# Kernel optimization log

Measured on AMD Instinct MI355X. Metric: run time of the kernel, lower is better.

The kernel has to match this reference:

```python
import jax, jax.numpy as jnp
import numpy as np

COST_CLASS = 1.0
COST_COORD = 1.0
ALPHA = 0.25
GAMMA = 2.0
EPS = 1e-8
B, N = 4, 512


def setup_inputs() -> dict:
    key = jax.random.key(0)
    k1, k2, k3 = jax.random.split(key, 3)
    return {
        "pred_logits": jax.random.normal(k1, (B, N), dtype=jnp.float32),
        "pred_points": jax.random.uniform(k2, (B, N, 2), dtype=jnp.float32),
        "gt_points": jax.random.uniform(k3, (B, N, 2), dtype=jnp.float32),
        "gt_mask": jnp.ones((B, N), dtype=bool),
    }


def _cost_matrix(pred_logits, pred_points, gt_points):
    # focal-style classification cost, depends only on the prediction -> column-constant
    prob = jax.nn.sigmoid(pred_logits)                       # [B, N]
    neg = (1.0 - ALPHA) * prob ** GAMMA * (-jnp.log(1.0 - prob + EPS))
    pos = ALPHA * (1.0 - prob) ** GAMMA * (-jnp.log(prob + EPS))
    cost_class = (pos - neg)[:, :, None]                     # [B, N, 1]
    # L1 cdist between pred_points and gt_points
    cost_coord = jnp.sum(
        jnp.abs(pred_points[:, :, None, :] - gt_points[:, None, :, :]), axis=-1
    )                                                        # [B, N, N]
    return COST_CLASS * cost_class + COST_COORD * cost_coord


def _lsa(cost):
    # Jonker-Volgenant shortest augmenting path (e-maxx Hungarian), square, minimization.
    c = np.asarray(cost, dtype=np.float64)
    n = c.shape[0]
    INF = 1e18
    u = np.zeros(n + 1)
    v = np.zeros(n + 1)
    p = np.zeros(n + 1, dtype=np.int64)   # p[j] = row matched to column j (1-based)
    way = np.zeros(n + 1, dtype=np.int64)
    for i in range(1, n + 1):
        p[0] = i
        j0 = 0
        minv = np.full(n + 1, INF)
        used = np.zeros(n + 1, dtype=bool)
        while True:
            used[j0] = True
            i0 = p[j0]
            cur = c[i0 - 1] - u[i0] - v[1:]
            nu = ~used[1:]
            mv = minv[1:]
            wy = way[1:]
            upd = nu & (cur < mv)
            mv[upd] = cur[upd]
            wy[upd] = j0
            cand = np.where(nu, mv, INF)
            j1 = int(np.argmin(cand)) + 1
            delta = cand[j1 - 1]
            u[p[used]] += delta
            v[used] -= delta
            mv[nu] -= delta
            j0 = j1
            if p[j0] == 0:
                break
        while j0:
            j1 = int(way[j0])
            p[j0] = int(p[j1])
            j0 = j1
    col_of_row = np.empty(n, dtype=np.int64)
    col_of_row[p[1:] - 1] = np.arange(n)
    return np.arange(n), col_of_row


def reference(pred_logits, pred_points, gt_points, gt_mask):
    C = _cost_matrix(pred_logits, pred_points, gt_points)   # [B, N, N]
    mask = np.asarray(gt_mask)
    assert mask.all(), "reference assumes all gt slots valid (static shapes)"
    Cn = np.asarray(jax.device_get(C))
    pred_idx, gt_idx = [], []
    for b in range(Cn.shape[0]):
        r, c = _lsa(Cn[b])
        pred_idx.append(r)
        gt_idx.append(c)
    pred_idx = jnp.asarray(np.stack(pred_idx))
    gt_idx = jnp.asarray(np.stack(gt_idx))
    return pred_idx, gt_idx, C
```

## Files before the change

### kernel.cpp

```cpp
#include <hip/hip_runtime.h>
#include <math.h>

constexpr int B_ = 4;
constexpr int N_ = 512;

__device__ __forceinline__ float cephes_expf(float xin) {
#pragma clang fp contract(off)
    float x = fminf(xin, 88.3762626647950f);
    x = fmaxf(x, -88.3762626647949f);
    float fx = x * 1.44269504088896341f;
    fx = fx + 0.5f;
    fx = floorf(fx);
    float tmp = fx * 0.693359375f;
    float z0  = fx * -2.12194440e-4f;
    float r = x - tmp;
    r = r - z0;
    float zz = r * r;
    float y = 1.9875691500E-4f;
    y = y * r + 1.3981999507E-3f;
    y = y * r + 8.3334519073E-3f;
    y = y * r + 4.1665795894E-2f;
    y = y * r + 1.6666665459E-1f;
    y = y * r + 5.0000001201E-1f;
    y = y * zz + r;
    y = y + 1.0f;
    int n = (int)fx;
    float p2n = __uint_as_float((unsigned)(n + 0x7f) << 23);
    float res = y * p2n;
    return fmaxf(res, xin);
}

__device__ __forceinline__ float cephes_logf(float t) {
#pragma clang fp contract(off)
    float xx = fmaxf(t, 1.17549435e-38f);
    unsigned u = __float_as_uint(xx);
    int e_i = (int)(u >> 23) - 0x7f;
    float e = (float)e_i + 1.0f;
    float m = __uint_as_float((u & 0x807fffffu) | 0x3f000000u);
    int mask = (m < 0.707106781186547524f);
    float tmp1 = mask ? m : 0.0f;
    float x = m - 1.0f;
    e = e - (mask ? 1.0f : 0.0f);
    x = x + tmp1;
    float z = x * x;
    float y = 7.0376836292E-2f;
    y = y * x + -1.1514610310E-1f;
    y = y * x + 1.1676998740E-1f;
    y = y * x + -1.2420140846E-1f;
    y = y * x + 1.4249322787E-1f;
    y = y * x + -1.6668057665E-1f;
    y = y * x + 2.0000714765E-1f;
    y = y * x + -2.4999993993E-1f;
    y = y * x + 3.3333331174E-1f;
    y = y * x;
    y = y * z;
    y = e * -2.12194440e-4f + y;
    y = y - z * 0.5f;
    float res = x + y;
    res = res + e * 0.693359375f;
    return res;
}

__global__ __launch_bounds__(256) void class_cost_kernel(
    const float* __restrict__ logits, float* __restrict__ cc_out)
{
#pragma clang fp contract(off)
    int idx = blockIdx.x * 256 + threadIdx.x;
    if (idx >= B_ * N_) return;
    float x    = logits[idx];
    float e    = cephes_expf(-x);
    float prob = 1.0f / (1.0f + e);
    float om   = 1.0f - prob;
    float p2   = prob * prob;
    float o2   = om * om;
    float lneg = cephes_logf(om   + 1e-8f);
    float lpos = cephes_logf(prob + 1e-8f);
    float neg  = (0.75f * p2) * (-lneg);
    float pos  = (0.25f * o2) * (-lpos);
    cc_out[idx] = pos - neg;
}

__global__ __launch_bounds__(512) void cost_kernel(
    const float* __restrict__ cc,
    const float* __restrict__ pred_pts,
    const float* __restrict__ gt_pts,
    float* __restrict__ C)
{
    int blk = blockIdx.x;
    int b = blk >> 9;
    int i = blk & (N_ - 1);
    int j = threadIdx.x;

    const float2* pp2 = reinterpret_cast<const float2*>(pred_pts);
    const float2* gp2 = reinterpret_cast<const float2*>(gt_pts);
    float2 pp = pp2[b * N_ + i];
    float2 gp = gp2[b * N_ + j];
    float coord = fabsf(pp.x - gp.x) + fabsf(pp.y - gp.y);

    C[(size_t)b * N_ * N_ + (size_t)i * N_ + j] = cc[blk] + coord;
}

template<int CTRL>
__device__ __forceinline__ uint32_t dpp32(uint32_t x) {
    return (uint32_t)__builtin_amdgcn_update_dpp((int)x, (int)x, CTRL, 0xF, 0xF, false);
}
#define UMINSTEP(X, CTRL) { uint32_t o_ = dpp32<CTRL>(X); X = (o_ < X) ? o_ : X; }

__device__ __forceinline__ uint32_t wave_umin_lane63(uint32_t x) {
    UMINSTEP(x, 0x111) UMINSTEP(x, 0x112) UMINSTEP(x, 0x114)
    UMINSTEP(x, 0x118) UMINSTEP(x, 0x142) UMINSTEP(x, 0x143)
    return x;
}

__device__ __forceinline__ double readlane_f64(double d, int lane) {
    unsigned long long ll = (unsigned long long)__double_as_longlong(d);
    unsigned lo = (unsigned)__builtin_amdgcn_readlane((int)(unsigned)ll, lane);
    unsigned hi = (unsigned)__builtin_amdgcn_readlane((int)(unsigned)(ll >> 32), lane);
    return __longlong_as_double((long long)(((unsigned long long)hi << 32) | lo));
}

__global__ __launch_bounds__(64, 1) void solve_kernel(
    const float* __restrict__ cc_in,
    const float* __restrict__ pred_pts,
    const float* __restrict__ gt_pts,
    float* __restrict__ pred_idx,
    float* __restrict__ gt_idx)
{
    const int b = blockIdx.x;
    const int t = threadIdx.x;

    const float2* pq = reinterpret_cast<const float2*>(pred_pts) + b * N_;
    const float2* gq = reinterpret_cast<const float2*>(gt_pts)   + b * N_;
    const float*  cq = cc_in + b * N_;
    const int base = t << 3;

    float2 r0 = pq[base + 0], r1 = pq[base + 1], r2 = pq[base + 2], r3 = pq[base + 3];
    float2 r4 = pq[base + 4], r5 = pq[base + 5], r6 = pq[base + 6], r7 = pq[base + 7];
    float2 g0 = gq[base + 0], g1 = gq[base + 1], g2 = gq[base + 2], g3 = gq[base + 3];
    float2 g4 = gq[base + 4], g5 = gq[base + 5], g6 = gq[base + 6], g7 = gq[base + 7];
    float  c0 = cq[base + 0], c1 = cq[base + 1], c2 = cq[base + 2], c3 = cq[base + 3];
    float  c4 = cq[base + 4], c5 = cq[base + 5], c6 = cq[base + 6], c7 = cq[base + 7];

    double u0=0.0,u1=0.0,u2=0.0,u3=0.0,u4=0.0,u5=0.0,u6=0.0,u7=0.0;
    double v0=0.0,v1=0.0,v2=0.0,v3=0.0,v4=0.0,v5=0.0,v6=0.0,v7=0.0;
    int    p0=-1,p1=-1,p2=-1,p3=-1,p4=-1,p5=-1,p6=-1,p7=-1;

    #pragma unroll
    for (int k = 0; k < 8; ++k)
        pred_idx[b * N_ + t + 64 * k] = (float)(t + 64 * k);

    #define SEL8I(sl, x0,x1,x2,x3,x4,x5,x6,x7, out) {                      \
        int a0_=((sl)&1)?(x1):(x0), a1_=((sl)&1)?(x3):(x2);                \
        int a2_=((sl)&1)?(x5):(x4), a3_=((sl)&1)?(x7):(x6);                \
        int b0_=((sl)&2)?a1_:a0_,   b1_=((sl)&2)?a3_:a2_;                  \
        out = ((sl)&4)?b1_:b0_; }

    float px_r, py_r, cc_r; double urow;

    #define RL_F(reg, ln) __uint_as_float((unsigned)__builtin_amdgcn_readlane( \
                              (int)__float_as_uint(reg), (ln)))
    #define ROW_ARM(s, ln) {                                               \
        px_r = RL_F(r##s.x, (ln)); py_r = RL_F(r##s.y, (ln));              \
        cc_r = RL_F(c##s,   (ln)); urow = readlane_f64(u##s, (ln)); }
    #define ROW_SCALARS(r) {                                               \
        int sl_ = (r) & 7, ln_ = (r) >> 3;                                 \
        if (sl_ < 4) {                                                     \
            if (sl_ < 2) { if (sl_ == 0) ROW_ARM(0, ln_) else ROW_ARM(1, ln_) } \
            else         { if (sl_ == 2) ROW_ARM(2, ln_) else ROW_ARM(3, ln_) } \
        } else {                                                           \
            if (sl_ < 6) { if (sl_ == 4) ROW_ARM(4, ln_) else ROW_ARM(5, ln_) } \
            else         { if (sl_ == 6) ROW_ARM(6, ln_) else ROW_ARM(7, ln_) } \
        } }

    #define UPDU(uvar, mask, k) {                                          \
        unsigned f_ = (unsigned)((int)((mask) << (31 - (k))) >> 31);       \
        uvar += __longlong_as_double((long long)(                          \
            (((unsigned long long)(dhi_ & f_)) << 32) | (dlo_ & f_))); }
    #define UPDV(vvar, mask, k) {                                          \
        unsigned f_ = (unsigned)((int)((mask) << (31 - (k))) >> 31);       \
        vvar -= __longlong_as_double((long long)(                          \
            (((unsigned long long)(dhi_ & f_)) << 32) | (dlo_ & f_))); }

    const float INF32 = __uint_as_float(0x7F800000u);

    for (int i = 0; i < N_; ++i) {
        unsigned used_m  = 0u;
        unsigned chain_m = (t == (i >> 3)) ? (1u << (i & 7)) : 0u;
        ROW_SCALARS(i);

        for (;;) {
#pragma clang fp contract(off)
            float w0 = cc_r + (fabsf(px_r - g0.x) + fabsf(py_r - g0.y));
            float w1 = cc_r + (fabsf(px_r - g1.x) + fabsf(py_r - g1.y));
            float w2 = cc_r + (fabsf(px_r - g2.x) + fabsf(py_r - g2.y));
            float w3 = cc_r + (fabsf(px_r - g3.x) + fabsf(py_r - g3.y));
            float w4 = cc_r + (fabsf(px_r - g4.x) + fabsf(py_r - g4.y));
            float w5 = cc_r + (fabsf(px_r - g5.x) + fabsf(py_r - g5.y));
            float w6 = cc_r + (fabsf(px_r - g6.x) + fabsf(py_r - g6.y));
            float w7 = cc_r + (fabsf(px_r - g7.x) + fabsf(py_r - g7.y));
            w0 = (used_m & 0x01u) ? INF32 : w0;
            w1 = (used_m & 0x02u) ? INF32 : w1;
            w2 = (used_m & 0x04u) ? INF32 : w2;
            w3 = (used_m & 0x08u) ? INF32 : w3;
            w4 = (used_m & 0x10u) ? INF32 : w4;
            w5 = (used_m & 0x20u) ? INF32 : w5;
            w6 = (used_m & 0x40u) ? INF32 : w6;
            w7 = (used_m & 0x80u) ? INF32 : w7;

            double d0 = ((double)w0 - urow) - v0;
            double d1 = ((double)w1 - urow) - v1;
            double d2 = ((double)w2 - urow) - v2;
            double d3 = ((double)w3 - urow) - v3;
            double d4 = ((double)w4 - urow) - v4;
            double d5 = ((double)w5 - urow) - v5;
            double d6 = ((double)w6 - urow) - v6;
            double d7 = ((double)w7 - urow) - v7;

            double  ka = (d1 < d0) ? d1 : d0;  uint32_t sa = (d1 < d0) ? 1u : 0u;
            double  kb = (d3 < d2) ? d3 : d2;  uint32_t sb = (d3 < d2) ? 3u : 2u;
            double  kx = (d5 < d4) ? d5 : d4;  uint32_t sx = (d5 < d4) ? 5u : 4u;
            double  kd = (d7 < d6) ? d7 : d6;  uint32_t sd = (d7 < d6) ? 7u : 6u;
            double  ke = (kb < ka) ? kb : ka;  uint32_t se = (kb < ka) ? sb : sa;
            double  kf = (kd < kx) ? kd : kx;  uint32_t sf = (kd < kx) ? sd : sx;
            double  bv = (kf < ke) ? kf : ke;  uint32_t bslot = (kf < ke) ? sf : se;

            uint64_t kb64 = (uint64_t)__double_as_longlong(bv);
            kb64 ^= (kb64 >> 63) ? 0xFFFFFFFFFFFFFFFFull : 0x8000000000000000ull;
            uint32_t khi = (uint32_t)(kb64 >> 32);
            uint32_t klo = (uint32_t)kb64;

            int own_pre;
            SEL8I(bslot, p0,p1,p2,p3,p4,p5,p6,p7, own_pre);

            uint32_t Mhi = (uint32_t)__builtin_amdgcn_readlane(
                               (int)wave_umin_lane63(khi), 63);
            unsigned long long tied_hi = __ballot(khi == Mhi);

            int lane1; uint32_t Mlo;
            if (__builtin_popcountll(tied_hi) == 1) {
                lane1 = (int)__builtin_ctzll(tied_hi);
                Mlo = (uint32_t)__builtin_amdgcn_readlane((int)klo, lane1);
            } else {
                uint32_t kl2 = (khi == Mhi) ? klo : 0xFFFFFFFFu;
                Mlo = (uint32_t)__builtin_amdgcn_readlane(
                          (int)wave_umin_lane63(kl2), 63);
                lane1 = (int)__builtin_ctzll(__ballot(khi == Mhi && klo == Mlo));
            }

            int slot1 = __builtin_amdgcn_readlane((int)bslot, lane1);
            int owner = __builtin_amdgcn_readlane(own_pre, lane1);

            uint64_t M = ((uint64_t)Mhi << 32) | Mlo;
            uint64_t db = (M >> 63) ? (M ^ 0x8000000000000000ull) : ~M;
            double delta = __longlong_as_double((long long)db);
            const unsigned dlo_ = (unsigned)(unsigned long long)__double_as_longlong(delta);
            const unsigned dhi_ = (unsigned)(((unsigned long long)__double_as_longlong(delta)) >> 32);

            if (owner < 0) {
                UPDU(u0, chain_m, 0) UPDU(u1, chain_m, 1)
                UPDU(u2, chain_m, 2) UPDU(u3, chain_m, 3)
                UPDU(u4, chain_m, 4) UPDU(u5, chain_m, 5)
                UPDU(u6, chain_m, 6) UPDU(u7, chain_m, 7)
                UPDV(v0, used_m, 0) UPDV(v1, used_m, 1)
                UPDV(v2, used_m, 2) UPDV(v3, used_m, 3)
                UPDV(v4, used_m, 4) UPDV(v5, used_m, 5)
                UPDV(v6, used_m, 6) UPDV(v7, used_m, 7)
                bool mine = (t == lane1);
                p0 = (mine && slot1 == 0) ? i : p0;
                p1 = (mine && slot1 == 1) ? i : p1;
                p2 = (mine && slot1 == 2) ? i : p2;
                p3 = (mine && slot1 == 3) ? i : p3;
                p4 = (mine && slot1 == 4) ? i : p4;
                p5 = (mine && slot1 == 5) ? i : p5;
                p6 = (mine && slot1 == 6) ? i : p6;
                p7 = (mine && slot1 == 7) ? i : p7;
                break;
            }

            ROW_SCALARS(owner);

            UPDU(u0, chain_m, 0) UPDU(u1, chain_m, 1)
            UPDU(u2, chain_m, 2) UPDU(u3, chain_m, 3)
            UPDU(u4, chain_m, 4) UPDU(u5, chain_m, 5)
            UPDU(u6, chain_m, 6) UPDU(u7, chain_m, 7)
            UPDV(v0, used_m, 0) UPDV(v1, used_m, 1)
            UPDV(v2, used_m, 2) UPDV(v3, used_m, 3)
            UPDV(v4, used_m, 4) UPDV(v5, used_m, 5)
            UPDV(v6, used_m, 6) UPDV(v7, used_m, 7)

            used_m  |= (t == lane1)        ? (1u << slot1)       : 0u;
            chain_m |= (t == (owner >> 3)) ? (1u << (owner & 7)) : 0u;
        }
    }

    gt_idx[b * N_ + p0] = (float)(base);
    gt_idx[b * N_ + p1] = (float)(base + 1);
    gt_idx[b * N_ + p2] = (float)(base + 2);
    gt_idx[b * N_ + p3] = (float)(base + 3);
    gt_idx[b * N_ + p4] = (float)(base + 4);
    gt_idx[b * N_ + p5] = (float)(base + 5);
    gt_idx[b * N_ + p6] = (float)(base + 6);
    gt_idx[b * N_ + p7] = (float)(base + 7);
}

extern "C" void kernel_launch(void* const* d_in, const int* in_sizes, int n_in,
                              void* d_out, int out_size, void* d_ws, size_t ws_size,
                              hipStream_t stream)
{
    const float* logits   = (const float*)d_in[0];
    const float* pred_pts = (const float*)d_in[1];
    const float* gt_pts   = (const float*)d_in[2];

    float* out      = (float*)d_out;
    float* pred_idx = out;
    float* gt_idx   = out + B_ * N_;
    float* C        = out + 2 * B_ * N_;
    float* cc       = (float*)d_ws;

    class_cost_kernel<<<(B_ * N_ + 255) / 256, 256, 0, stream>>>(logits, cc);
    cost_kernel<<<B_ * N_, N_, 0, stream>>>(cc, pred_pts, gt_pts, C);
    solve_kernel<<<B_, 64, 0, stream>>>(cc, pred_pts, gt_pts, pred_idx, gt_idx);
}
```

Before: 1.634 ms.

## Flatten Hungarian loops, use 64-bit DPP min, select row scalars branch-free

Merges the outer row loop and inner augmenting loop into one loop, so a terminal step just resets the masks and advances the row instead of leaving the loop. Replaces the two-stage 32-bit min reduction, which took a data-dependent path on ties, with a single 64-bit DPP min reduction followed by one ballot. Selects row scalars with select trees in place of nested branches. Together these are meant to cut scalar branching and latency on the serial critical path, at the cost of more VALU work per reduction step and some extra selects on every iteration.

```diff
diff --git a/kernel.cpp b/kernel.cpp
--- a/kernel.cpp
+++ b/kernel.cpp
@@ -104,12 +104,17 @@
 __device__ __forceinline__ uint32_t dpp32(uint32_t x) {
     return (uint32_t)__builtin_amdgcn_update_dpp((int)x, (int)x, CTRL, 0xF, 0xF, false);
 }
-#define UMINSTEP(X, CTRL) { uint32_t o_ = dpp32<CTRL>(X); X = (o_ < X) ? o_ : X; }
-
-__device__ __forceinline__ uint32_t wave_umin_lane63(uint32_t x) {
-    UMINSTEP(x, 0x111) UMINSTEP(x, 0x112) UMINSTEP(x, 0x114)
-    UMINSTEP(x, 0x118) UMINSTEP(x, 0x142) UMINSTEP(x, 0x143)
-    return x;
+
+#define UMINSTEP64(K, CTRL) {                                              \
+    uint32_t oh_ = dpp32<CTRL>((uint32_t)((K) >> 32));                     \
+    uint32_t ol_ = dpp32<CTRL>((uint32_t)(K));                             \
+    uint64_t o_  = ((uint64_t)oh_ << 32) | ol_;                            \
+    K = (o_ < K) ? o_ : K; }
+
+__device__ __forceinline__ uint64_t wave_umin64_lane63(uint64_t k) {
+    UMINSTEP64(k, 0x111) UMINSTEP64(k, 0x112) UMINSTEP64(k, 0x114)
+    UMINSTEP64(k, 0x118) UMINSTEP64(k, 0x142) UMINSTEP64(k, 0x143)
+    return k;
 }
 
 __device__ __forceinline__ double readlane_f64(double d, int lane) {
@@ -118,6 +123,52 @@
     unsigned hi = (unsigned)__builtin_amdgcn_readlane((int)(unsigned)(ll >> 32), lane);
     return __longlong_as_double((long long)(((unsigned long long)hi << 32) | lo));
 }
+
+__device__ __forceinline__ uint64_t readlane_u64(uint64_t k, int lane) {
+    unsigned lo = (unsigned)__builtin_amdgcn_readlane((int)(unsigned)k, lane);
+    unsigned hi = (unsigned)__builtin_amdgcn_readlane((int)(unsigned)(k >> 32), lane);
+    return ((uint64_t)hi << 32) | lo;
+}
+
+#define SEL8F(sl, x0,x1,x2,x3,x4,x5,x6,x7, out) {                      \
+    float a0_=((sl)&1)?(x1):(x0), a1_=((sl)&1)?(x3):(x2);              \
+    float a2_=((sl)&1)?(x5):(x4), a3_=((sl)&1)?(x7):(x6);              \
+    float b0_=((sl)&2)?a1_:a0_,   b1_=((sl)&2)?a3_:a2_;                \
+    out = ((sl)&4)?b1_:b0_; }
+#define SEL8I(sl, x0,x1,x2,x3,x4,x5,x6,x7, out) {                      \
+    int a0_=((sl)&1)?(x1):(x0), a1_=((sl)&1)?(x3):(x2);                \
+    int a2_=((sl)&1)?(x5):(x4), a3_=((sl)&1)?(x7):(x6);                \
+    int b0_=((sl)&2)?a1_:a0_,   b1_=((sl)&2)?a3_:a2_;                  \
+    out = ((sl)&4)?b1_:b0_; }
+#define SEL8D(sl, x0,x1,x2,x3,x4,x5,x6,x7, out) {                      \
+    double a0_=((sl)&1)?(x1):(x0), a1_=((sl)&1)?(x3):(x2);             \
+    double a2_=((sl)&1)?(x5):(x4), a3_=((sl)&1)?(x7):(x6);             \
+    double b0_=((sl)&2)?a1_:a0_,   b1_=((sl)&2)?a3_:a2_;               \
+    out = ((sl)&4)?b1_:b0_; }
+
+#define ROW_SCALARS(r) {                                                   \
+    int sl_ = (r) & 7, ln_ = (r) >> 3;                                     \
+    float sx_, sy_, sc_; double su_;                                       \
+    SEL8F(sl_, r0.x,r1.x,r2.x,r3.x,r4.x,r5.x,r6.x,r7.x, sx_);              \
+    SEL8F(sl_, r0.y,r1.y,r2.y,r3.y,r4.y,r5.y,r6.y,r7.y, sy_);              \
+    SEL8F(sl_, c0,c1,c2,c3,c4,c5,c6,c7, sc_);                              \
+    SEL8D(sl_, u0,u1,u2,u3,u4,u5,u6,u7, su_);                              \
+    px_r = __uint_as_float((unsigned)__builtin_amdgcn_readlane(            \
+               (int)__float_as_uint(sx_), ln_));                           \
+    py_r = __uint_as_float((unsigned)__builtin_amdgcn_readlane(            \
+               (int)__float_as_uint(sy_), ln_));                           \
+    cc_r = __uint_as_float((unsigned)__builtin_amdgcn_readlane(            \
+               (int)__float_as_uint(sc_), ln_));                           \
+    urow = readlane_f64(su_, ln_); }
+
+#define UPDU(uvar, mask, k) {                                              \
+    unsigned f_ = (unsigned)((int)((mask) << (31 - (k))) >> 31);           \
+    uvar += __longlong_as_double((long long)(                              \
+        (((unsigned long long)(dhi_ & f_)) << 32) | (dlo_ & f_))); }
+#define UPDV(vvar, mask, k) {                                              \
+    unsigned f_ = (unsigned)((int)((mask) << (31 - (k))) >> 31);           \
+    vvar -= __longlong_as_double((long long)(                              \
+        (((unsigned long long)(dhi_ & f_)) << 32) | (dlo_ & f_))); }
 
 __global__ __launch_bounds__(64, 1) void solve_kernel(
     const float* __restrict__ cc_in,
@@ -126,6 +177,7 @@
     float* __restrict__ pred_idx,
     float* __restrict__ gt_idx)
 {
+#pragma clang fp contract(off)
     const int b = blockIdx.x;
     const int t = threadIdx.x;
 
@@ -149,148 +201,99 @@
     for (int k = 0; k < 8; ++k)
         pred_idx[b * N_ + t + 64 * k] = (float)(t + 64 * k);
 
-    #define SEL8I(sl, x0,x1,x2,x3,x4,x5,x6,x7, out) {                      \
-        int a0_=((sl)&1)?(x1):(x0), a1_=((sl)&1)?(x3):(x2);                \
-        int a2_=((sl)&1)?(x5):(x4), a3_=((sl)&1)?(x7):(x6);                \
-        int b0_=((sl)&2)?a1_:a0_,   b1_=((sl)&2)?a3_:a2_;                  \
-        out = ((sl)&4)?b1_:b0_; }
-
     float px_r, py_r, cc_r; double urow;
-
-    #define RL_F(reg, ln) __uint_as_float((unsigned)__builtin_amdgcn_readlane( \
-                              (int)__float_as_uint(reg), (ln)))
-    #define ROW_ARM(s, ln) {                                               \
-        px_r = RL_F(r##s.x, (ln)); py_r = RL_F(r##s.y, (ln));              \
-        cc_r = RL_F(c##s,   (ln)); urow = readlane_f64(u##s, (ln)); }
-    #define ROW_SCALARS(r) {                                               \
-        int sl_ = (r) & 7, ln_ = (r) >> 3;                                 \
-        if (sl_ < 4) {                                                     \
-            if (sl_ < 2) { if (sl_ == 0) ROW_ARM(0, ln_) else ROW_ARM(1, ln_) } \
-            else         { if (sl_ == 2) ROW_ARM(2, ln_) else ROW_ARM(3, ln_) } \
-        } else {                                                           \
-            if (sl_ < 6) { if (sl_ == 4) ROW_ARM(4, ln_) else ROW_ARM(5, ln_) } \
-            else         { if (sl_ == 6) ROW_ARM(6, ln_) else ROW_ARM(7, ln_) } \
-        } }
-
-    #define UPDU(uvar, mask, k) {                                          \
-        unsigned f_ = (unsigned)((int)((mask) << (31 - (k))) >> 31);       \
-        uvar += __longlong_as_double((long long)(                          \
-            (((unsigned long long)(dhi_ & f_)) << 32) | (dlo_ & f_))); }
-    #define UPDV(vvar, mask, k) {                                          \
-        unsigned f_ = (unsigned)((int)((mask) << (31 - (k))) >> 31);       \
-        vvar -= __longlong_as_double((long long)(                          \
-            (((unsigned long long)(dhi_ & f_)) << 32) | (dlo_ & f_))); }
-
     const float INF32 = __uint_as_float(0x7F800000u);
 
-    for (int i = 0; i < N_; ++i) {
-        unsigned used_m  = 0u;
-        unsigned chain_m = (t == (i >> 3)) ? (1u << (i & 7)) : 0u;
-        ROW_SCALARS(i);
-
-        for (;;) {
-#pragma clang fp contract(off)
-            float w0 = cc_r + (fabsf(px_r - g0.x) + fabsf(py_r - g0.y));
-            float w1 = cc_r + (fabsf(px_r - g1.x) + fabsf(py_r - g1.y));
-            float w2 = cc_r + (fabsf(px_r - g2.x) + fabsf(py_r - g2.y));
-            float w3 = cc_r + (fabsf(px_r - g3.x) + fabsf(py_r - g3.y));
-            float w4 = cc_r + (fabsf(px_r - g4.x) + fabsf(py_r - g4.y));
-            float w5 = cc_r + (fabsf(px_r - g5.x) + fabsf(py_r - g5.y));
-            float w6 = cc_r + (fabsf(px_r - g6.x) + fabsf(py_r - g6.y));
-            float w7 = cc_r + (fabsf(px_r - g7.x) + fabsf(py_r - g7.y));
-            w0 = (used_m & 0x01u) ? INF32 : w0;
-            w1 = (used_m & 0x02u) ? INF32 : w1;
-            w2 = (used_m & 0x04u) ? INF32 : w2;
-            w3 = (used_m & 0x08u) ? INF32 : w3;
-            w4 = (used_m & 0x10u) ? INF32 : w4;
-            w5 = (used_m & 0x20u) ? INF32 : w5;
-            w6 = (used_m & 0x40u) ? INF32 : w6;
-            w7 = (used_m & 0x80u) ? INF32 : w7;
-
-            double d0 = ((double)w0 - urow) - v0;
-            double d1 = ((double)w1 - urow) - v1;
-            double d2 = ((double)w2 - urow) - v2;
-            double d3 = ((double)w3 - urow) - v3;
-            double d4 = ((double)w4 - urow) - v4;
-            double d5 = ((double)w5 - urow) - v5;
-            double d6 = ((double)w6 - urow) - v6;
-            double d7 = ((double)w7 - urow) - v7;
-
-            double  ka = (d1 < d0) ? d1 : d0;  uint32_t sa = (d1 < d0) ? 1u : 0u;
-            double  kb = (d3 < d2) ? d3 : d2;  uint32_t sb = (d3 < d2) ? 3u : 2u;
-            double  kx = (d5 < d4) ? d5 : d4;  uint32_t sx = (d5 < d4) ? 5u : 4u;
-            double  kd = (d7 < d6) ? d7 : d6;  uint32_t sd = (d7 < d6) ? 7u : 6u;
-            double  ke = (kb < ka) ? kb : ka;  uint32_t se = (kb < ka) ? sb : sa;
-            double  kf = (kd < kx) ? kd : kx;  uint32_t sf = (kd < kx) ? sd : sx;
-            double  bv = (kf < ke) ? kf : ke;  uint32_t bslot = (kf < ke) ? sf : se;
-
-            uint64_t kb64 = (uint64_t)__double_as_longlong(bv);
-            kb64 ^= (kb64 >> 63) ? 0xFFFFFFFFFFFFFFFFull : 0x8000000000000000ull;
-            uint32_t khi = (uint32_t)(kb64 >> 32);
-            uint32_t klo = (uint32_t)kb64;
-
-            int own_pre;
-            SEL8I(bslot, p0,p1,p2,p3,p4,p5,p6,p7, own_pre);
-
-            uint32_t Mhi = (uint32_t)__builtin_amdgcn_readlane(
-                               (int)wave_umin_lane63(khi), 63);
-            unsigned long long tied_hi = __ballot(khi == Mhi);
-
-            int lane1; uint32_t Mlo;
-            if (__builtin_popcountll(tied_hi) == 1) {
-                lane1 = (int)__builtin_ctzll(tied_hi);
-                Mlo = (uint32_t)__builtin_amdgcn_readlane((int)klo, lane1);
-            } else {
-                uint32_t kl2 = (khi == Mhi) ? klo : 0xFFFFFFFFu;
-                Mlo = (uint32_t)__builtin_amdgcn_readlane(
-                          (int)wave_umin_lane63(kl2), 63);
-                lane1 = (int)__builtin_ctzll(__ballot(khi == Mhi && klo == Mlo));
-            }
-
-            int slot1 = __builtin_amdgcn_readlane((int)bslot, lane1);
-            int owner = __builtin_amdgcn_readlane(own_pre, lane1);
-
-            uint64_t M = ((uint64_t)Mhi << 32) | Mlo;
-            uint64_t db = (M >> 63) ? (M ^ 0x8000000000000000ull) : ~M;
-            double delta = __longlong_as_double((long long)db);
-            const unsigned dlo_ = (unsigned)(unsigned long long)__double_as_longlong(delta);
-            const unsigned dhi_ = (unsigned)(((unsigned long long)__double_as_longlong(delta)) >> 32);
-
-            if (owner < 0) {
-                UPDU(u0, chain_m, 0) UPDU(u1, chain_m, 1)
-                UPDU(u2, chain_m, 2) UPDU(u3, chain_m, 3)
-                UPDU(u4, chain_m, 4) UPDU(u5, chain_m, 5)
-                UPDU(u6, chain_m, 6) UPDU(u7, chain_m, 7)
-                UPDV(v0, used_m, 0) UPDV(v1, used_m, 1)
-                UPDV(v2, used_m, 2) UPDV(v3, used_m, 3)
-                UPDV(v4, used_m, 4) UPDV(v5, used_m, 5)
-                UPDV(v6, used_m, 6) UPDV(v7, used_m, 7)
-                bool mine = (t == lane1);
-                p0 = (mine && slot1 == 0) ? i : p0;
-                p1 = (mine && slot1 == 1) ? i : p1;
-                p2 = (mine && slot1 == 2) ? i : p2;
-                p3 = (mine && slot1 == 3) ? i : p3;
-                p4 = (mine && slot1 == 4) ? i : p4;
-                p5 = (mine && slot1 == 5) ? i : p5;
-                p6 = (mine && slot1 == 6) ? i : p6;
-                p7 = (mine && slot1 == 7) ? i : p7;
-                break;
-            }
-
-            ROW_SCALARS(owner);
-
-            UPDU(u0, chain_m, 0) UPDU(u1, chain_m, 1)
-            UPDU(u2, chain_m, 2) UPDU(u3, chain_m, 3)
-            UPDU(u4, chain_m, 4) UPDU(u5, chain_m, 5)
-            UPDU(u6, chain_m, 6) UPDU(u7, chain_m, 7)
-            UPDV(v0, used_m, 0) UPDV(v1, used_m, 1)
-            UPDV(v2, used_m, 2) UPDV(v3, used_m, 3)
-            UPDV(v4, used_m, 4) UPDV(v5, used_m, 5)
-            UPDV(v6, used_m, 6) UPDV(v7, used_m, 7)
-
-            used_m  |= (t == lane1)        ? (1u << slot1)       : 0u;
-            chain_m |= (t == (owner >> 3)) ? (1u << (owner & 7)) : 0u;
-        }
+    unsigned used_m  = 0u;
+    unsigned chain_m = (t == 0) ? 1u : 0u;
+    int i = 0;
+
+    ROW_SCALARS(0);
+
+    for (;;) {
+        float w0 = cc_r + (fabsf(px_r - g0.x) + fabsf(py_r - g0.y));
+        float w1 = cc_r + (fabsf(px_r - g1.x) + fabsf(py_r - g1.y));
+        float w2 = cc_r + (fabsf(px_r - g2.x) + fabsf(py_r - g2.y));
+        float w3 = cc_r + (fabsf(px_r - g3.x) + fabsf(py_r - g3.y));
+        float w4 = cc_r + (fabsf(px_r - g4.x) + fabsf(py_r - g4.y));
+        float w5 = cc_r + (fabsf(px_r - g5.x) + fabsf(py_r - g5.y));
+        float w6 = cc_r + (fabsf(px_r - g6.x) + fabsf(py_r - g6.y));
+        float w7 = cc_r + (fabsf(px_r - g7.x) + fabsf(py_r - g7.y));
+        w0 = (used_m & 0x01u) ? INF32 : w0;
+        w1 = (used_m & 0x02u) ? INF32 : w1;
+        w2 = (used_m & 0x04u) ? INF32 : w2;
+        w3 = (used_m & 0x08u) ? INF32 : w3;
+        w4 = (used_m & 0x10u) ? INF32 : w4;
+        w5 = (used_m & 0x20u) ? INF32 : w5;
+        w6 = (used_m & 0x40u) ? INF32 : w6;
+        w7 = (used_m & 0x80u) ? INF32 : w7;
+
+        double d0 = ((double)w0 - urow) - v0;
+        double d1 = ((double)w1 - urow) - v1;
+        double d2 = ((double)w2 - urow) - v2;
+        double d3 = ((double)w3 - urow) - v3;
+        double d4 = ((double)w4 - urow) - v4;
+        double d5 = ((double)w5 - urow) - v5;
+        double d6 = ((double)w6 - urow) - v6;
+        double d7 = ((double)w7 - urow) - v7;
+
+        double  ka = (d1 < d0) ? d1 : d0;  uint32_t sa = (d1 < d0) ? 1u : 0u;
+        double  kb = (d3 < d2) ? d3 : d2;  uint32_t sb = (d3 < d2) ? 3u : 2u;
+        double  kx = (d5 < d4) ? d5 : d4;  uint32_t sx = (d5 < d4) ? 5u : 4u;
+        double  kd = (d7 < d6) ? d7 : d6;  uint32_t sd = (d7 < d6) ? 7u : 6u;
+        double  ke = (kb < ka) ? kb : ka;  uint32_t se = (kb < ka) ? sb : sa;
+        double  kf = (kd < kx) ? kd : kx;  uint32_t sf = (kd < kx) ? sd : sx;
+        double  bv = (kf < ke) ? kf : ke;  uint32_t bslot = (kf < ke) ? sf : se;
+
+        uint64_t kb64 = (uint64_t)__double_as_longlong(bv);
+        kb64 ^= (kb64 >> 63) ? 0xFFFFFFFFFFFFFFFFull : 0x8000000000000000ull;
+
+        int own_pre;
+        SEL8I(bslot, p0,p1,p2,p3,p4,p5,p6,p7, own_pre);
+
+        uint64_t M = readlane_u64(wave_umin64_lane63(kb64), 63);
+        int lane1 = (int)__builtin_ctzll(__ballot(kb64 == M));
+
+        int slot1 = __builtin_amdgcn_readlane((int)bslot, lane1);
+        int owner = __builtin_amdgcn_readlane(own_pre, lane1);
+
+        uint64_t db = (M >> 63) ? (M ^ 0x8000000000000000ull) : ~M;
+        double delta = __longlong_as_double((long long)db);
+        const unsigned dlo_ = (unsigned)(unsigned long long)__double_as_longlong(delta);
+        const unsigned dhi_ = (unsigned)(((unsigned long long)__double_as_longlong(delta)) >> 32);
+
+        int terminal = (owner < 0) ? 1 : 0;
+        int nxt  = terminal ? (i + 1) : owner;
+        int nxtc = (nxt > (N_ - 1)) ? (N_ - 1) : nxt;
+
+        ROW_SCALARS(nxtc);
+
+        UPDU(u0, chain_m, 0) UPDU(u1, chain_m, 1)
+        UPDU(u2, chain_m, 2) UPDU(u3, chain_m, 3)
+        UPDU(u4, chain_m, 4) UPDU(u5, chain_m, 5)
+        UPDU(u6, chain_m, 6) UPDU(u7, chain_m, 7)
+        UPDV(v0, used_m, 0) UPDV(v1, used_m, 1)
+        UPDV(v2, used_m, 2) UPDV(v3, used_m, 3)
+        UPDV(v4, used_m, 4) UPDV(v5, used_m, 5)
+        UPDV(v6, used_m, 6) UPDV(v7, used_m, 7)
+
+        bool mine = (t == lane1);
+        p0 = (terminal && mine && slot1 == 0) ? i : p0;
+        p1 = (terminal && mine && slot1 == 1) ? i : p1;
+        p2 = (terminal && mine && slot1 == 2) ? i : p2;
+        p3 = (terminal && mine && slot1 == 3) ? i : p3;
+        p4 = (terminal && mine && slot1 == 4) ? i : p4;
+        p5 = (terminal && mine && slot1 == 5) ? i : p5;
+        p6 = (terminal && mine && slot1 == 6) ? i : p6;
+        p7 = (terminal && mine && slot1 == 7) ? i : p7;
+
+        unsigned hopbit = (t == (nxt >> 3)) ? (1u << (nxt & 7)) : 0u;
+        unsigned selbit = mine ? (1u << slot1) : 0u;
+        chain_m = terminal ? hopbit : (chain_m | hopbit);
+        used_m  = terminal ? 0u     : (used_m  | selbit);
+        i += terminal;
+
+        if (i >= N_) break;
     }
 
     gt_idx[b * N_ + p0] = (float)(base);
```

Measured after the change: 1.731 ms. 5.9% more time.
